# Kernel tuning notes

Hardware: AMD Instinct MI355X
Metric: run time of the kernel (lower is better)

The kernel has to match this reference:

```python
import jax, jax.numpy as jnp
import numpy as np

N_NODES = 32768
N_EDGES = 131072
BATCH = 512
SEQ_LEN = 1000
VOCAB = 26  # vocab_size=25 + 1 padding row
EMB = 128


def _bn(x, g, b):
    # BatchNorm1d forward with batch statistics (training-mode math), eps=1e-5
    m = x.mean(0)
    v = x.var(0)
    return g * (x - m) * jax.lax.rsqrt(v + 1e-5) + b


def _gcn(x, src, dst, W, b, n):
    deg = 1.0 + jax.ops.segment_sum(jnp.ones(src.shape[0], x.dtype), dst, num_segments=n)
    dis = jax.lax.rsqrt(deg)
    xw = x @ W
    msg = xw[src] * (dis[src] * dis[dst])[:, None]
    agg = jax.ops.segment_sum(msg, dst, num_segments=n) + xw * (dis * dis)[:, None]
    return agg + b


def _conv1d(x, k, b, pad):
    # x: [B, C_in, L], k: [C_out, C_in, K]
    y = jax.lax.conv_general_dilated(x, k, (1,), [(pad, pad)],
                                     dimension_numbers=('NCH', 'OIH', 'NCH'))
    return y + b[None, :, None]


def setup_inputs() -> dict:
    key = jax.random.key(0)
    ks = jax.random.split(key, 32)
    f = lambda i, shape, s=0.1: (jax.random.normal(ks[i], shape, dtype=jnp.float32) * s)
    inp = {
        'x': jax.random.normal(ks[0], (N_NODES, 5), dtype=jnp.float32),
        'edge_index': jax.random.randint(ks[1], (2, N_EDGES), 0, N_NODES, dtype=jnp.int32),
        'batch': jnp.sort(jax.random.randint(ks[2], (N_NODES,), 0, BATCH, dtype=jnp.int32)),
        'protein_seq': jax.random.randint(ks[3], (BATCH, SEQ_LEN), 0, VOCAB, dtype=jnp.int32),
        # GCN weights
        'W1': f(4, (5, 64)), 'b1': f(5, (64,)),
        'g1': jnp.ones((64,)), 'bt1': jnp.zeros((64,)),
        'W2': f(6, (64, 128)), 'b2': f(7, (128,)),
        'g2': jnp.ones((128,)), 'bt2': jnp.zeros((128,)),
        'W3': f(8, (128, 128)), 'b3': f(9, (128,)),
        'g3': jnp.ones((128,)), 'bt3': jnp.zeros((128,)),
        # protein embedding (row 0 = padding_idx, zeroed)
        'emb': f(10, (VOCAB, EMB)).at[0].set(0.0),
        # protein convs
        'ck1': f(11, (32, 128, 4)), 'cb1': f(12, (32,)),
        'ck2': f(13, (64, 32, 6)), 'cb2': f(14, (64,)),
        'ck3': f(15, (96, 64, 8)), 'cb3': f(16, (96,)),
        'fw1': f(17, (224, 512)), 'fb1': f(18, (512,)),
        'fw2': f(19, (512, 256)), 'fb2': f(20, (256,)),
        'fw3': f(21, (256, 1)), 'fb3': f(22, (1,)),
    }
    return inp


def reference(x, edge_index, batch, protein_seq,
              W1, b1, g1, bt1, W2, b2, g2, bt2, W3, b3, g3, bt3,
              emb, ck1, cb1, ck2, cb2, ck3, cb3,
              fw1, fb1, fw2, fb2, fw3, fb3):
    src, dst = edge_index[0], edge_index[1]
    relu = jax.nn.relu
    # Drug GNN encoder
    h = relu(_bn(_gcn(x, src, dst, W1, b1, N_NODES), g1, bt1))
    h = relu(_bn(_gcn(h, src, dst, W2, b2, N_NODES), g2, bt2))
    h = relu(_bn(_gcn(h, src, dst, W3, b3, N_NODES), g3, bt3))
    cnt = jax.ops.segment_sum(jnp.ones(N_NODES, h.dtype), batch, num_segments=BATCH)
    drug_emb = jax.ops.segment_sum(h, batch, num_segments=BATCH) / jnp.maximum(cnt, 1.0)[:, None]
    # Protein CNN encoder
    e = emb[protein_seq]                    # [B, L, 128]
    p = jnp.transpose(e, (0, 2, 1))         # [B, 128, L]
    p = relu(_conv1d(p, ck1, cb1, 1))       # [B, 32, 999]
    p = relu(_conv1d(p, ck2, cb2, 2))       # [B, 64, 998]
    p = relu(_conv1d(p, ck3, cb3, 3))       # [B, 96, 997]
    prot_emb = p.max(axis=2)                # [B, 96]
    c = jnp.concatenate([drug_emb, prot_emb], axis=1)  # [B, 224]
    c = relu(c @ fw1 + fb1)
    c = relu(c @ fw2 + fb2)
    out = (c @ fw3 + fb3)[:, 0]             # [B]
    return out
```

## Files before the change

### kernel.cpp

```cpp
#include <hip/hip_runtime.h>

#define NN 32768
#define NE 131072
#define NB 512
#define SL 1000

using bf16x8 = __attribute__((ext_vector_type(8))) short;
using f32x4  = __attribute__((ext_vector_type(4))) float;

static __device__ __forceinline__ unsigned short f2b(float f) {
  union { float f; unsigned u; } x; x.f = f;
  unsigned r = x.u + 0x7fffu + ((x.u >> 16) & 1u);
  return (unsigned short)(r >> 16);
}

static __device__ __forceinline__ void bn_from_raw(float sum, float ssq, float g, float b,
                                                   float& sc, float& sh) {
  float m = sum / 32768.f;
  float v = ssq / 32768.f - m * m;
  sc = g * rsqrtf(v + 1e-5f);
  sh = b - m * sc;
}

__global__ void k_degprep(const int* __restrict__ dst, int* __restrict__ degi,
                          const float* __restrict__ emb, const float* __restrict__ ck1,
                          const float* __restrict__ ck2, const float* __restrict__ ck3,
                          unsigned short* __restrict__ emb_bf, unsigned short* __restrict__ wt1,
                          unsigned short* __restrict__ wt2, unsigned short* __restrict__ wt3) {
  int gid = blockIdx.x * 256 + threadIdx.x;
  atomicAdd(&degi[dst[gid]], 1);
  int idx = gid;
  if (idx < 3328) {
    emb_bf[idx] = f2b(emb[idx]);
  } else if (idx < 3328 + 16384) {
    int i = idx - 3328;
    int kt = i >> 12, co = (i >> 7) & 31, ci = i & 127;
    wt1[i] = f2b(ck1[co * 512 + ci * 4 + kt]);
  } else if (idx < 3328 + 16384 + 12288) {
    int i = idx - 3328 - 16384;
    int kt = i >> 11, co = (i >> 5) & 63, ci = i & 31;
    wt2[i] = f2b(ck2[co * 192 + ci * 6 + kt]);
  } else if (idx < 3328 + 16384 + 12288 + 49152) {
    int i = idx - 3328 - 16384 - 12288;
    int kt = i / 6144, co = (i >> 6) % 96, ci = i & 63;
    wt3[i] = f2b(ck3[co * 512 + ci * 8 + kt]);
  }
}

__global__ void k_scan(const int* __restrict__ degi, int* __restrict__ base,
                       int* __restrict__ cursor, float* __restrict__ dis) {
  __shared__ int part[1024];
  int tid = threadIdx.x;
  int v[32];
  int s = 0;
  int lo = tid * 32;
#pragma unroll
  for (int i = 0; i < 32; ++i) { v[i] = degi[lo + i]; s += v[i]; }
  part[tid] = s;
  __syncthreads();
  for (int off = 1; off < 1024; off <<= 1) {
    int val = (tid >= off) ? part[tid - off] : 0;
    __syncthreads();
    part[tid] += val;
    __syncthreads();
  }
  int run = (tid > 0) ? part[tid - 1] : 0;
#pragma unroll
  for (int i = 0; i < 32; ++i) {
    base[lo + i] = run;
    cursor[lo + i] = run;
    dis[lo + i] = rsqrtf(1.0f + (float)v[i]);
    run += v[i];
  }
  if (tid == 1023) base[NN] = run;
}

__global__ void k_fill(const int* __restrict__ src, const int* __restrict__ dst,
                       int* __restrict__ cursor, unsigned short* __restrict__ csr_src, int E) {
  int e = blockIdx.x * 256 + threadIdx.x;
  if (e < E) {
    int d = dst[e];
    int pos = atomicAdd(&cursor[d], 1);
    csr_src[pos] = (unsigned short)src[e];
  }
}

__launch_bounds__(256)
__global__ void k_gfc1s(const float* __restrict__ x, const float* __restrict__ dis,
                        const int* __restrict__ base, const unsigned short* __restrict__ csr_src,
                        const float* __restrict__ W1, float* __restrict__ out,
                        float* __restrict__ st) {
  __shared__ float sW[5][64];
  __shared__ float a5[256][6];
  __shared__ float red[16][64];
  int tid = threadIdx.x;
  for (int i = tid; i < 320; i += 256) sW[i >> 6][i & 63] = W1[i];
  int n = blockIdx.x * 256 + tid;
  float dn = dis[n];
  float s2 = dn * dn;
  const float* xn = x + (long)n * 5;
  float a0 = xn[0] * s2, a1 = xn[1] * s2, a2 = xn[2] * s2, a3 = xn[3] * s2, a4 = xn[4] * s2;
  int b0 = base[n], b1 = base[n + 1];
  int sNext = (b0 < b1) ? csr_src[b0] : 0;
  for (int j = b0; j < b1; ++j) {
    int s = sNext;
    if (j + 1 < b1) sNext = csr_src[j + 1];
    float coef = dis[s] * dn;
    const float* xs = x + (long)s * 5;
    a0 += xs[0] * coef; a1 += xs[1] * coef; a2 += xs[2] * coef;
    a3 += xs[3] * coef; a4 += xs[4] * coef;
  }
  a5[tid][0] = a0; a5[tid][1] = a1; a5[tid][2] = a2; a5[tid][3] = a3; a5[tid][4] = a4;
  __syncthreads();
  int co = (tid & 15) * 4, strip = tid >> 4;
  float4 s4 = {0.f, 0.f, 0.f, 0.f}, ss4 = {0.f, 0.f, 0.f, 0.f};
  for (int i = 0; i < 16; ++i) {
    int nl = strip * 16 + i;
    long nn = (long)blockIdx.x * 256 + nl;
    float4 acc = {0.f, 0.f, 0.f, 0.f};
#pragma unroll
    for (int ci = 0; ci < 5; ++ci) {
      float av = a5[nl][ci];
      acc.x += av * sW[ci][co];     acc.y += av * sW[ci][co + 1];
      acc.z += av * sW[ci][co + 2]; acc.w += av * sW[ci][co + 3];
    }
    *(float4*)&out[nn * 64 + co] = acc;
    s4.x += acc.x; s4.y += acc.y; s4.z += acc.z; s4.w += acc.w;
    ss4.x += acc.x * acc.x; ss4.y += acc.y * acc.y;
    ss4.z += acc.z * acc.z; ss4.w += acc.w * acc.w;
  }
  *(float4*)&red[strip][co] = s4;
  __syncthreads();
  if (tid < 64) {
    float t = 0.f;
#pragma unroll
    for (int s = 0; s < 16; ++s) t += red[s][tid];
    atomicAdd(&st[tid], t);
  }
  __syncthreads();
  *(float4*)&red[strip][co] = ss4;
  __syncthreads();
  if (tid < 64) {
    float t = 0.f;
#pragma unroll
    for (int s = 0; s < 16; ++s) t += red[s][tid];
    atomicAdd(&st[64 + tid], t);
  }
}

template<int C>
__launch_bounds__(256)
__global__ void k_gbngather(const float* __restrict__ in, const float* __restrict__ dis,
                            const int* __restrict__ base, const unsigned short* __restrict__ csr_src,
                            const float* __restrict__ st, const float* __restrict__ g,
                            const float* __restrict__ bt, float* __restrict__ out) {
  constexpr int TPN = C / 4;
  int t = blockIdx.x * 256 + threadIdx.x;
  int n = t / TPN;
  int c = (t % TPN) * 4;
  float4 sum4 = *(const float4*)&st[c];
  float4 ssq4 = *(const float4*)&st[C + c];
  float4 gg = *(const float4*)&g[c];
  float4 bb = *(const float4*)&bt[c];
  float4 sc4, sh4;
  bn_from_raw(sum4.x, ssq4.x, gg.x, bb.x, sc4.x, sh4.x);
  bn_from_raw(sum4.y, ssq4.y, gg.y, bb.y, sc4.y, sh4.y);
  bn_from_raw(sum4.z, ssq4.z, gg.z, bb.z, sc4.z, sh4.z);
  bn_from_raw(sum4.w, ssq4.w, gg.w, bb.w, sc4.w, sh4.w);
  float dn = dis[n];
  float s2 = dn * dn;
  float4 a = *(const float4*)&in[(long)n * C + c];
  float4 acc;
  acc.x = fmaxf(a.x * sc4.x + sh4.x, 0.f) * s2;
  acc.y = fmaxf(a.y * sc4.y + sh4.y, 0.f) * s2;
  acc.z = fmaxf(a.z * sc4.z + sh4.z, 0.f) * s2;
  acc.w = fmaxf(a.w * sc4.w + sh4.w, 0.f) * s2;
  int b0 = base[n], b1 = base[n + 1];
  int sNext = (b0 < b1) ? csr_src[b0] : 0;
  for (int j = b0; j < b1; ++j) {
    int s = sNext;
    if (j + 1 < b1) sNext = csr_src[j + 1];
    float coef = dis[s] * dn;
    float4 vv = *(const float4*)&in[(long)s * C + c];
    acc.x += fmaxf(vv.x * sc4.x + sh4.x, 0.f) * coef;
    acc.y += fmaxf(vv.y * sc4.y + sh4.y, 0.f) * coef;
    acc.z += fmaxf(vv.z * sc4.z + sh4.z, 0.f) * coef;
    acc.w += fmaxf(vv.w * sc4.w + sh4.w, 0.f) * coef;
  }
  *(float4*)&out[(long)n * C + c] = acc;
}

template<int C_OUT, int K, int TN, bool RELU, bool BIAS, bool STATS>
__launch_bounds__(256)
__global__ void k_fc4(const float* __restrict__ in, const float* __restrict__ W,
                      const float* __restrict__ bias, float* __restrict__ out,
                      float* __restrict__ st, int N) {
  constexpr int CO4 = C_OUT / 4;
  constexpr int GPB = 256 / CO4;
  int g = blockIdx.x * GPB + threadIdx.x / CO4;
  long n0 = (long)g * TN;
  if (!STATS && n0 >= N) return;
  int co = (threadIdx.x % CO4) * 4;
  float4 acc[TN];
  float4 b4 = {0.f, 0.f, 0.f, 0.f};
  if (BIAS) b4 = *(const float4*)&bias[co];
#pragma unroll
  for (int t = 0; t < TN; ++t) acc[t] = b4;
  for (int ci = 0; ci < K; ci += 4) {
    float4 w0 = *(const float4*)&W[(long)(ci + 0) * C_OUT + co];
    float4 w1 = *(const float4*)&W[(long)(ci + 1) * C_OUT + co];
    float4 w2 = *(const float4*)&W[(long)(ci + 2) * C_OUT + co];
    float4 w3 = *(const float4*)&W[(long)(ci + 3) * C_OUT + co];
#pragma unroll
    for (int t = 0; t < TN; ++t) {
      float4 a = *(const float4*)&in[(n0 + t) * K + ci];
      acc[t].x += a.x * w0.x; acc[t].y += a.x * w0.y; acc[t].z += a.x * w0.z; acc[t].w += a.x * w0.w;
      acc[t].x += a.y * w1.x; acc[t].y += a.y * w1.y; acc[t].z += a.y * w1.z; acc[t].w += a.y * w1.w;
      acc[t].x += a.z * w2.x; acc[t].y += a.z * w2.y; acc[t].z += a.z * w2.z; acc[t].w += a.z * w2.w;
      acc[t].x += a.w * w3.x; acc[t].y += a.w * w3.y; acc[t].z += a.w * w3.z; acc[t].w += a.w * w3.w;
    }
  }
  float4 s4 = {0.f, 0.f, 0.f, 0.f}, ss4 = {0.f, 0.f, 0.f, 0.f};
#pragma unroll
  for (int t = 0; t < TN; ++t) {
    float4 o = acc[t];
    if (RELU) {
      o.x = fmaxf(o.x, 0.f); o.y = fmaxf(o.y, 0.f);
      o.z = fmaxf(o.z, 0.f); o.w = fmaxf(o.w, 0.f);
    }
    *(float4*)&out[(n0 + t) * C_OUT + co] = o;
    if (STATS) {
      s4.x += o.x; s4.y += o.y; s4.z += o.z; s4.w += o.w;
      ss4.x += o.x * o.x; ss4.y += o.y * o.y;
      ss4.z += o.z * o.z; ss4.w += o.w * o.w;
    }
  }
  if (STATS) {
    __shared__ float red2[GPB][C_OUT];
    int grp = threadIdx.x / CO4;
    *(float4*)&red2[grp][co] = s4;
    __syncthreads();
    if (threadIdx.x < C_OUT) {
      float t = 0.f;
#pragma unroll
      for (int s = 0; s < GPB; ++s) t += red2[s][threadIdx.x];
      atomicAdd(&st[threadIdx.x], t);
    }
    __syncthreads();
    *(float4*)&red2[grp][co] = ss4;
    __syncthreads();
    if (threadIdx.x < C_OUT) {
      float t = 0.f;
#pragma unroll
      for (int s = 0; s < GPB; ++s) t += red2[s][threadIdx.x];
      atomicAdd(&st[C_OUT + threadIdx.x], t);
    }
  }
}

__launch_bounds__(256)
__global__ void k_reg(const float* __restrict__ cbuf,
                      const float* __restrict__ fw1, const float* __restrict__ fb1,
                      const float* __restrict__ fw2, const float* __restrict__ fb2,
                      const float* __restrict__ fw3, const float* __restrict__ fb3,
                      float* __restrict__ out) {
  __shared__ float cin[224];
  __shared__ float h1[512];
  __shared__ float h2[256];
  __shared__ float red[4];
  int b = blockIdx.x, t = threadIdx.x;
  if (t < 224) cin[t] = cbuf[b * 224 + t];
  __syncthreads();
  {
    float a0 = fb1[t], a1 = fb1[t + 256];
    for (int ci = 0; ci < 224; ++ci) {
      float av = cin[ci];
      a0 += av * fw1[ci * 512 + t];
      a1 += av * fw1[ci * 512 + t + 256];
    }
    h1[t] = fmaxf(a0, 0.f);
    h1[t + 256] = fmaxf(a1, 0.f);
  }
  __syncthreads();
  {
    float a = fb2[t];
    for (int ci = 0; ci < 512; ++ci) a += h1[ci] * fw2[ci * 256 + t];
    h2[t] = fmaxf(a, 0.f);
  }
  __syncthreads();
  {
    float p = h2[t] * fw3[t];
#pragma unroll
    for (int off = 32; off > 0; off >>= 1) p += __shfl_down(p, off, 64);
    if ((t & 63) == 0) red[t >> 6] = p;
    __syncthreads();
    if (t == 0) out[b] = red[0] + red[1] + red[2] + red[3] + fb3[0];
  }
}

__launch_bounds__(256, 3)
__global__ void conv_mfma(const int* __restrict__ seq, const unsigned short* __restrict__ emb_bf,
                          const unsigned short* __restrict__ wt1g, const float* __restrict__ cb1,
                          const unsigned short* __restrict__ wt2g, const float* __restrict__ cb2,
                          const unsigned short* __restrict__ wt3g, const float* __restrict__ cb3,
                          const float* __restrict__ agg, const float* __restrict__ st3,
                          const float* __restrict__ g3, const float* __restrict__ bt3,
                          const int* __restrict__ batch, float* __restrict__ outmax) {
  __shared__ __align__(16) unsigned short s_w[12288];
  __shared__ __align__(16) unsigned short s_c1[4864];
  __shared__ __align__(16) unsigned short s_c2[9216];
  __shared__ int s_tok[152];
  __shared__ int s_max[96];

  int tid = threadIdx.x;
  int b = blockIdx.y;

  if (blockIdx.x == 8) {
    __shared__ int s_lo, s_hi;
    if (tid == 0) {
      int lo = 0, hi = NN;
      while (lo < hi) { int m = (lo + hi) >> 1; if (batch[m] < b) lo = m + 1; else hi = m; }
      s_lo = lo;
      hi = NN;
      while (lo < hi) { int m = (lo + hi) >> 1; if (batch[m] <= b) lo = m + 1; else hi = m; }
      s_hi = lo;
    }
    __syncthreads();
    if (tid < 128) {
      int lo = s_lo, hi = s_hi, c = tid;
      float sc, sh;
      bn_from_raw(st3[c], st3[128 + c], g3[c], bt3[c], sc, sh);
      float s = 0.f;
      for (int n = lo; n < hi; ++n) s += fmaxf(agg[(long)n * 128 + c] * sc + sh, 0.f);
      outmax[b * 224 + c] = s / fmaxf((float)(hi - lo), 1.0f);
    }
    return;
  }

  int t0 = blockIdx.x * 128;

  if (tid < 96) s_max[tid] = 0;
  if (tid < 152) {
    int p = t0 - 6 + tid;
    s_tok[tid] = (p >= 0 && p < SL) ? seq[b * SL + p] : 0;
  }
  if (tid < 128) ((int*)(s_c1 + 144 * 32))[tid] = 0;

  {
    int v0 = tid, v1 = tid + 256;
    *(bf16x8*)&s_w[(v0 >> 4) * 128 + ((((v0 >> 4) ^ v0) & 15) << 3)] = *(const bf16x8*)(wt1g + v0 * 8);
    *(bf16x8*)&s_w[(v1 >> 4) * 128 + ((((v1 >> 4) ^ v1) & 15) << 3)] = *(const bf16x8*)(wt1g + v1 * 8);
  }
  __syncthreads();

  int lane = tid & 63, wave = tid >> 6;
  int l15 = lane & 15, quad = lane >> 4;

  {
    int mt0 = wave, mt1 = wave + 4;
    f32x4 acc0[2], acc1[2], acc2[2];
#pragma unroll
    for (int nt = 0; nt < 2; ++nt) {
      float bv = cb1[nt * 16 + l15];
      acc0[nt] = (f32x4){bv, bv, bv, bv};
      acc1[nt] = (f32x4){bv, bv, bv, bv};
      acc2[nt] = (f32x4){bv, bv, bv, bv};
    }
    for (int kt = 0; kt < 4; ++kt) {
      int bo = (kt & 1) * 4096;
      if (kt < 3) {
        int bo2 = 4096 - bo;
        const unsigned short* wsrc = wt1g + (kt + 1) * 4096;
        int v0 = tid, v1 = tid + 256;
        *(bf16x8*)&s_w[bo2 + (v0 >> 4) * 128 + ((((v0 >> 4) ^ v0) & 15) << 3)] = *(const bf16x8*)(wsrc + v0 * 8);
        *(bf16x8*)&s_w[bo2 + (v1 >> 4) * 128 + ((((v1 >> 4) ^ v1) & 15) << 3)] = *(const bf16x8*)(wsrc + v1 * 8);
      }
      const unsigned short* e0 = emb_bf + s_tok[mt0 * 16 + l15 + kt] * 128 + quad * 8;
      const unsigned short* e1 = emb_bf + s_tok[mt1 * 16 + l15 + kt] * 128 + quad * 8;
#pragma unroll
      for (int cb = 0; cb < 4; ++cb) {
        bf16x8 a0 = *(const bf16x8*)(e0 + cb * 32);
        bf16x8 a1 = *(const bf16x8*)(e1 + cb * 32);
#pragma unroll
        for (int nt = 0; nt < 2; ++nt) {
          bf16x8 bf = *(const bf16x8*)&s_w[bo + (nt * 16 + l15) * 128 + (((cb * 4 + quad) ^ l15) << 3)];
          acc0[nt] = __builtin_amdgcn_mfma_f32_16x16x32_bf16(a0, bf, acc0[nt], 0, 0, 0);
          acc1[nt] = __builtin_amdgcn_mfma_f32_16x16x32_bf16(a1, bf, acc1[nt], 0, 0, 0);
        }
      }
      if (wave == 0) {
        const unsigned short* e2 = emb_bf + s_tok[128 + l15 + kt] * 128 + quad * 8;
#pragma unroll
        for (int cb = 0; cb < 4; ++cb) {
          bf16x8 a2 = *(const bf16x8*)(e2 + cb * 32);
#pragma unroll
          for (int nt = 0; nt < 2; ++nt) {
            bf16x8 bf = *(const bf16x8*)&s_w[bo + (nt * 16 + l15) * 128 + (((cb * 4 + quad) ^ l15) << 3)];
            acc2[nt] = __builtin_amdgcn_mfma_f32_16x16x32_bf16(a2, bf, acc2[nt], 0, 0, 0);
          }
        }
      }
      __syncthreads();
    }
#pragma unroll
    for (int nt = 0; nt < 2; ++nt) {
      int co = nt * 16 + l15;
#pragma unroll
      for (int r = 0; r < 4; ++r) {
        {
          int m = mt0 * 16 + quad * 4 + r;
          int l1 = t0 - 5 + m;
          unsigned short hv = f2b(fmaxf(acc0[nt][r], 0.f));
          s_c1[m * 32 + ((((co >> 3) ^ m) & 3) << 3) + (co & 7)] = (l1 >= 0 && l1 < 999) ? hv : (unsigned short)0;
        }
        {
          int m = mt1 * 16 + quad * 4 + r;
          int l1 = t0 - 5 + m;
          unsigned short hv = f2b(fmaxf(acc1[nt][r], 0.f));
          s_c1[m * 32 + ((((co >> 3) ^ m) & 3) << 3) + (co & 7)] = (l1 >= 0 && l1 < 999) ? hv : (unsigned short)0;
        }
      }
    }
    if (wave == 0) {
#pragma unroll
      for (int nt = 0; nt < 2; ++nt) {
        int co = nt * 16 + l15;
#pragma unroll
        for (int r = 0; r < 4; ++r) {
          int m = 128 + quad * 4 + r;
          int l1 = t0 - 5 + m;
          unsigned short hv = f2b(fmaxf(acc2[nt][r], 0.f));
          s_c1[m * 32 + ((((co >> 3) ^ m) & 3) << 3) + (co & 7)] = (l1 >= 0 && l1 < 999) ? hv : (unsigned short)0;
        }
      }
    }
  }

  {
    bf16x8 w2t[6];
#pragma unroll
    for (int c = 0; c < 6; ++c) w2t[c] = *(const bf16x8*)(wt2g + (c * 256 + tid) * 8);
#pragma unroll
    for (int c = 0; c < 6; ++c) {
      int ch = c * 256 + tid;
      int row = ch >> 2;
      *(bf16x8*)&s_w[row * 32 + (((row ^ ch) & 3) << 3)] = w2t[c];
    }
    __syncthreads();
  }

  {
    int mt0 = wave, mt1 = wave + 4;
    f32x4 acc[2][4];
#pragma unroll
    for (int nt = 0; nt < 4; ++nt) {
      float bv = cb2[nt * 16 + l15];
      acc[0][nt] = (f32x4){bv, bv, bv, bv};
      acc[1][nt] = (f32x4){bv, bv, bv, bv};
    }
    for (int kt = 0; kt < 6; ++kt) {
      int r0 = mt0 * 16 + l15 + kt, r1 = mt1 * 16 + l15 + kt;
      bf16x8 a0 = *(const bf16x8*)&s_c1[r0 * 32 + (((quad ^ r0) & 3) << 3)];
      bf16x8 a1 = *(const bf16x8*)&s_c1[r1 * 32 + (((quad ^ r1) & 3) << 3)];
#pragma unroll
      for (int nt = 0; nt < 4; ++nt) {
        int wr = kt * 64 + nt * 16 + l15;
        bf16x8 bf = *(const bf16x8*)&s_w[wr * 32 + (((quad ^ wr) & 3) << 3)];
        acc[0][nt] = __builtin_amdgcn_mfma_f32_16x16x32_bf16(a0, bf, acc[0][nt], 0, 0, 0);
        acc[1][nt] = __builtin_amdgcn_mfma_f32_16x16x32_bf16(a1, bf, acc[1][nt], 0, 0, 0);
      }
    }
#pragma unroll
    for (int mb = 0; mb < 2; ++mb) {
      int mt = mb ? mt1 : mt0;
#pragma unroll
      for (int nt = 0; nt < 4; ++nt) {
        int co = nt * 16 + l15;
#pragma unroll
        for (int r = 0; r < 4; ++r) {
          int m = mt * 16 + quad * 4 + r;
          int l2 = t0 - 3 + m;
          unsigned short hv = f2b(fmaxf(acc[mb][nt][r], 0.f));
          s_c2[m * 64 + ((((co >> 3) ^ m) & 7) << 3) + (co & 7)] = (l2 >= 0 && l2 < 998) ? hv : (unsigned short)0;
        }
      }
    }
    if (wave == 0) {
      f32x4 acc8[4];
#pragma unroll
      for (int nt = 0; nt < 4; ++nt) {
        float bv = cb2[nt * 16 + l15];
        acc8[nt] = (f32x4){bv, bv, bv, bv};
      }
      for (int kt = 0; kt < 6; ++kt) {
        int r0 = 128 + l15 + kt;
        bf16x8 a0 = *(const bf16x8*)&s_c1[r0 * 32 + (((quad ^ r0) & 3) << 3)];
#pragma unroll
        for (int nt = 0; nt < 4; ++nt) {
          int wr = kt * 64 + nt * 16 + l15;
          bf16x8 bf = *(const bf16x8*)&s_w[wr * 32 + (((quad ^ wr) & 3) << 3)];
          acc8[nt] = __builtin_amdgcn_mfma_f32_16x16x32_bf16(a0, bf, acc8[nt], 0, 0, 0);
        }
      }
#pragma unroll
      for (int nt = 0; nt < 4; ++nt) {
        int co = nt * 16 + l15;
#pragma unroll
        for (int r = 0; r < 4; ++r) {
          int m = 128 + quad * 4 + r;
          int l2 = t0 - 3 + m;
          unsigned short hv = f2b(fmaxf(acc8[nt][r], 0.f));
          s_c2[m * 64 + ((((co >> 3) ^ m) & 7) << 3) + (co & 7)] = (l2 >= 0 && l2 < 998) ? hv : (unsigned short)0;
        }
      }
    }
  }

  {
    bf16x8 w3t[3];
#pragma unroll
    for (int c = 0; c < 3; ++c) w3t[c] = *(const bf16x8*)(wt3g + (c * 256 + tid) * 8);
    __syncthreads();
#pragma unroll
    for (int c = 0; c < 3; ++c) {
      int ch = c * 256 + tid;
      int row = ch >> 3;
      *(bf16x8*)&s_w[row * 64 + (((row ^ ch) & 7) << 3)] = w3t[c];
    }
    __syncthreads();
  }

  {
    int mt0 = wave, mt1 = wave + 4;
    f32x4 acc[2][6];
#pragma unroll
    for (int nt = 0; nt < 6; ++nt) {
      float bv = cb3[nt * 16 + l15];
      acc[0][nt] = (f32x4){bv, bv, bv, bv};
      acc[1][nt] = (f32x4){bv, bv, bv, bv};
    }
    for (int kt = 0; kt < 8; ++kt) {
      bf16x8 w3t[3];
      if (kt < 7) {
#pragma unroll
        for (int c = 0; c < 3; ++c)
          w3t[c] = *(const bf16x8*)(wt3g + ((kt + 1) * 768 + c * 256 + tid) * 8);
      }
      int bo = (kt & 1) * 6144;
      int ra0 = mt0 * 16 + l15 + kt, ra1 = mt1 * 16 + l15 + kt;
#pragma unroll
      for (int cb = 0; cb < 2; ++cb) {
        bf16x8 a0 = *(const bf16x8*)&s_c2[ra0 * 64 + ((((cb * 4 + quad) ^ ra0) & 7) << 3)];
        bf16x8 a1 = *(const bf16x8*)&s_c2[ra1 * 64 + ((((cb * 4 + quad) ^ ra1) & 7) << 3)];
#pragma unroll
        for (int nt = 0; nt < 6; ++nt) {
          int wr = nt * 16 + l15;
          bf16x8 bf = *(const bf16x8*)&s_w[bo + wr * 64 + ((((cb * 4 + quad) ^ wr) & 7) << 3)];
          acc[0][nt] = __builtin_amdgcn_mfma_f32_16x16x32_bf16(a0, bf, acc[0][nt], 0, 0, 0);
          acc[1][nt] = __builtin_amdgcn_mfma_f32_16x16x32_bf16(a1, bf, acc[1][nt], 0, 0, 0);
        }
      }
      if (kt < 7) {
        int bo2 = 6144 - bo;
#pragma unroll
        for (int c = 0; c < 3; ++c) {
          int ch = c * 256 + tid;
          int row = ch >> 3;
          *(bf16x8*)&s_w[bo2 + row * 64 + (((row ^ ch) & 7) << 3)] = w3t[c];
        }
      }
      __syncthreads();
    }
#pragma unroll
    for (int nt = 0; nt < 6; ++nt) {
      int co = nt * 16 + l15;
      float mx = 0.f;
#pragma unroll
      for (int mb = 0; mb < 2; ++mb) {
        int mt = mb ? mt1 : mt0;
#pragma unroll
        for (int r = 0; r < 4; ++r) {
          int l3 = t0 + mt * 16 + quad * 4 + r;
          if (l3 < 997) mx = fmaxf(mx, acc[mb][nt][r]);
        }
      }
      atomicMax(&s_max[co], __float_as_int(mx));
    }
  }
  __syncthreads();
  if (tid < 96) atomicMax((int*)&outmax[b * 224 + 128 + tid], s_max[tid]);
}

extern "C" void kernel_launch(void* const* d_in, const int* in_sizes, int n_in,
                              void* d_out, int out_size, void* d_ws, size_t ws_size,
                              hipStream_t stream) {
  (void)in_sizes; (void)n_in; (void)out_size; (void)ws_size;
  const float* x = (const float*)d_in[0];
  const int* ei = (const int*)d_in[1];
  const int* batch = (const int*)d_in[2];
  const int* seq = (const int*)d_in[3];
  const float* W1 = (const float*)d_in[4];
  const float* g1 = (const float*)d_in[6];
  const float* bt1 = (const float*)d_in[7];
  const float* W2 = (const float*)d_in[8];
  const float* g2 = (const float*)d_in[10];
  const float* bt2 = (const float*)d_in[11];
  const float* W3 = (const float*)d_in[12];
  const float* g3 = (const float*)d_in[14];
  const float* bt3 = (const float*)d_in[15];
  const float* emb = (const float*)d_in[16];
  const float* ck1 = (const float*)d_in[17];
  const float* cb1 = (const float*)d_in[18];
  const float* ck2 = (const float*)d_in[19];
  const float* cb2 = (const float*)d_in[20];
  const float* ck3 = (const float*)d_in[21];
  const float* cb3 = (const float*)d_in[22];
  const float* fw1 = (const float*)d_in[23];
  const float* fb1 = (const float*)d_in[24];
  const float* fw2 = (const float*)d_in[25];
  const float* fb2 = (const float*)d_in[26];
  const float* fw3 = (const float*)d_in[27];
  const float* fb3 = (const float*)d_in[28];
  const int* src = ei;
  const int* dst = ei + NE;

  float* ws = (float*)d_ws;
  float* bufA = ws;
  float* bufB = ws + 4194304;
  float* dis = ws + 8388608;
  float* stats = ws + 8421376;
  float* cbuf = ws + 8422032;
  int* degi = (int*)(ws + 8536720);
  int* base = degi + NN;
  int* cursor = base + NN + 1;
  unsigned short* csr_src = (unsigned short*)(cursor + NN);
  unsigned short* emb_bf = (unsigned short*)(ws + 8700564);
  unsigned short* wt1 = emb_bf + 3328;
  unsigned short* wt2 = wt1 + 16384;
  unsigned short* wt3 = wt2 + 12288;
  float* out = (float*)d_out;

  hipMemsetAsync(stats, 0, (656 + 114688 + 32768) * sizeof(float), stream);

  k_degprep<<<NE / 256, 256, 0, stream>>>(dst, degi, emb, ck1, ck2, ck3, emb_bf, wt1, wt2, wt3);
  k_scan<<<1, 1024, 0, stream>>>(degi, base, cursor, dis);
  k_fill<<<NE / 256, 256, 0, stream>>>(src, dst, cursor, csr_src, NE);

  k_gfc1s<<<NN / 256, 256, 0, stream>>>(x, dis, base, csr_src, W1, bufA, stats);
  k_gbngather<64><<<NN * 16 / 256, 256, 0, stream>>>(bufA, dis, base, csr_src, stats, g1, bt1, bufB);
  k_fc4<128, 64, 4, false, false, true><<<1024, 256, 0, stream>>>(bufB, W2, nullptr, bufA, stats + 128, NN);
  k_gbngather<128><<<NN * 32 / 256, 256, 0, stream>>>(bufA, dis, base, csr_src, stats + 128, g2, bt2, bufB);
  k_fc4<128, 128, 4, false, false, true><<<1024, 256, 0, stream>>>(bufB, W3, nullptr, bufA, stats + 384, NN);

  conv_mfma<<<dim3(9, NB), 256, 0, stream>>>(seq, emb_bf, wt1, cb1, wt2, cb2, wt3, cb3,
                                             bufA, stats + 384, g3, bt3, batch, cbuf);

  k_reg<<<NB, 256, 0, stream>>>(cbuf, fw1, fb1, fw2, fb2, fw3, fb3, out);
}
```

Measured before the change: 431.2 us.

## Precompute embedding-by-conv1 weight table, replace conv1 MFMA with table lookups

Because the first conv runs on embeddings of only 26 tokens, the product of each token embedding with each conv1 tap is precomputed once in the prep kernel as a 26x4x32 fp32 table. Conv1 in the main kernel then sums four table rows per output position instead of running bf16 MFMAs over 128 input channels. This removes conv1 weight staging, MFMA work and syncs from every block, at the cost of a small serial dot-product loop in the prep kernel and gathers from a global table. Precision improves slightly since the table is kept in fp32.

```diff
diff --git a/kernel.cpp b/kernel.cpp
--- a/kernel.cpp
+++ b/kernel.cpp
@@ -26,7 +26,8 @@
                           const float* __restrict__ emb, const float* __restrict__ ck1,
                           const float* __restrict__ ck2, const float* __restrict__ ck3,
                           unsigned short* __restrict__ emb_bf, unsigned short* __restrict__ wt1,
-                          unsigned short* __restrict__ wt2, unsigned short* __restrict__ wt3) {
+                          unsigned short* __restrict__ wt2, unsigned short* __restrict__ wt3,
+                          float* __restrict__ e1) {
   int gid = blockIdx.x * 256 + threadIdx.x;
   atomicAdd(&degi[dst[gid]], 1);
   int idx = gid;
@@ -44,6 +45,14 @@
     int i = idx - 3328 - 16384 - 12288;
     int kt = i / 6144, co = (i >> 6) % 96, ci = i & 63;
     wt3[i] = f2b(ck3[co * 512 + ci * 8 + kt]);
+  } else if (idx < 3328 + 16384 + 12288 + 49152 + 3328) {
+    int i = idx - 81152;
+    int t = i >> 7, kt = (i >> 5) & 3, co = i & 31;
+    const float* er = emb + t * 128;
+    float s = 0.f;
+#pragma unroll 4
+    for (int ci = 0; ci < 128; ++ci) s += er[ci] * ck1[co * 512 + ci * 4 + kt];
+    e1[i] = s;
   }
 }
 
@@ -299,8 +308,8 @@
 }
 
 __launch_bounds__(256, 3)
-__global__ void conv_mfma(const int* __restrict__ seq, const unsigned short* __restrict__ emb_bf,
-                          const unsigned short* __restrict__ wt1g, const float* __restrict__ cb1,
+__global__ void conv_mfma(const int* __restrict__ seq, const float* __restrict__ e1g,
+                          const float* __restrict__ cb1,
                           const unsigned short* __restrict__ wt2g, const float* __restrict__ cb2,
                           const unsigned short* __restrict__ wt3g, const float* __restrict__ cb3,
                           const float* __restrict__ agg, const float* __restrict__ st3,
@@ -347,107 +356,54 @@
   if (tid < 128) ((int*)(s_c1 + 144 * 32))[tid] = 0;
 
   {
-    int v0 = tid, v1 = tid + 256;
-    *(bf16x8*)&s_w[(v0 >> 4) * 128 + ((((v0 >> 4) ^ v0) & 15) << 3)] = *(const bf16x8*)(wt1g + v0 * 8);
-    *(bf16x8*)&s_w[(v1 >> 4) * 128 + ((((v1 >> 4) ^ v1) & 15) << 3)] = *(const bf16x8*)(wt1g + v1 * 8);
-  }
-  __syncthreads();
-
-  int lane = tid & 63, wave = tid >> 6;
-  int l15 = lane & 15, quad = lane >> 4;
-
-  {
-    int mt0 = wave, mt1 = wave + 4;
-    f32x4 acc0[2], acc1[2], acc2[2];
-#pragma unroll
-    for (int nt = 0; nt < 2; ++nt) {
-      float bv = cb1[nt * 16 + l15];
-      acc0[nt] = (f32x4){bv, bv, bv, bv};
-      acc1[nt] = (f32x4){bv, bv, bv, bv};
-      acc2[nt] = (f32x4){bv, bv, bv, bv};
-    }
-    for (int kt = 0; kt < 4; ++kt) {
-      int bo = (kt & 1) * 4096;
-      if (kt < 3) {
-        int bo2 = 4096 - bo;
-        const unsigned short* wsrc = wt1g + (kt + 1) * 4096;
-        int v0 = tid, v1 = tid + 256;
-        *(bf16x8*)&s_w[bo2 + (v0 >> 4) * 128 + ((((v0 >> 4) ^ v0) & 15) << 3)] = *(const bf16x8*)(wsrc + v0 * 8);
-        *(bf16x8*)&s_w[bo2 + (v1 >> 4) * 128 + ((((v1 >> 4) ^ v1) & 15) << 3)] = *(const bf16x8*)(wsrc + v1 * 8);
-      }
-      const unsigned short* e0 = emb_bf + s_tok[mt0 * 16 + l15 + kt] * 128 + quad * 8;
-      const unsigned short* e1 = emb_bf + s_tok[mt1 * 16 + l15 + kt] * 128 + quad * 8;
-#pragma unroll
-      for (int cb = 0; cb < 4; ++cb) {
-        bf16x8 a0 = *(const bf16x8*)(e0 + cb * 32);
-        bf16x8 a1 = *(const bf16x8*)(e1 + cb * 32);
-#pragma unroll
-        for (int nt = 0; nt < 2; ++nt) {
-          bf16x8 bf = *(const bf16x8*)&s_w[bo + (nt * 16 + l15) * 128 + (((cb * 4 + quad) ^ l15) << 3)];
-          acc0[nt] = __builtin_amdgcn_mfma_f32_16x16x32_bf16(a0, bf, acc0[nt], 0, 0, 0);
-          acc1[nt] = __builtin_amdgcn_mfma_f32_16x16x32_bf16(a1, bf, acc1[nt], 0, 0, 0);
-        }
-      }
-      if (wave == 0) {
-        const unsigned short* e2 = emb_bf + s_tok[128 + l15 + kt] * 128 + quad * 8;
-#pragma unroll
-        for (int cb = 0; cb < 4; ++cb) {
-          bf16x8 a2 = *(const bf16x8*)(e2 + cb * 32);
-#pragma unroll
-          for (int nt = 0; nt < 2; ++nt) {
-            bf16x8 bf = *(const bf16x8*)&s_w[bo + (nt * 16 + l15) * 128 + (((cb * 4 + quad) ^ l15) << 3)];
-            acc2[nt] = __builtin_amdgcn_mfma_f32_16x16x32_bf16(a2, bf, acc2[nt], 0, 0, 0);
-          }
-        }
-      }
-      __syncthreads();
-    }
-#pragma unroll
-    for (int nt = 0; nt < 2; ++nt) {
-      int co = nt * 16 + l15;
-#pragma unroll
-      for (int r = 0; r < 4; ++r) {
-        {
-          int m = mt0 * 16 + quad * 4 + r;
-          int l1 = t0 - 5 + m;
-          unsigned short hv = f2b(fmaxf(acc0[nt][r], 0.f));
-          s_c1[m * 32 + ((((co >> 3) ^ m) & 3) << 3) + (co & 7)] = (l1 >= 0 && l1 < 999) ? hv : (unsigned short)0;
-        }
-        {
-          int m = mt1 * 16 + quad * 4 + r;
-          int l1 = t0 - 5 + m;
-          unsigned short hv = f2b(fmaxf(acc1[nt][r], 0.f));
-          s_c1[m * 32 + ((((co >> 3) ^ m) & 3) << 3) + (co & 7)] = (l1 >= 0 && l1 < 999) ? hv : (unsigned short)0;
-        }
-      }
-    }
-    if (wave == 0) {
-#pragma unroll
-      for (int nt = 0; nt < 2; ++nt) {
-        int co = nt * 16 + l15;
-#pragma unroll
-        for (int r = 0; r < 4; ++r) {
-          int m = 128 + quad * 4 + r;
-          int l1 = t0 - 5 + m;
-          unsigned short hv = f2b(fmaxf(acc2[nt][r], 0.f));
-          s_c1[m * 32 + ((((co >> 3) ^ m) & 3) << 3) + (co & 7)] = (l1 >= 0 && l1 < 999) ? hv : (unsigned short)0;
-        }
-      }
-    }
-  }
-
-  {
-    bf16x8 w2t[6];
-#pragma unroll
-    for (int c = 0; c < 6; ++c) w2t[c] = *(const bf16x8*)(wt2g + (c * 256 + tid) * 8);
 #pragma unroll
     for (int c = 0; c < 6; ++c) {
       int ch = c * 256 + tid;
       int row = ch >> 2;
-      *(bf16x8*)&s_w[row * 32 + (((row ^ ch) & 3) << 3)] = w2t[c];
-    }
-    __syncthreads();
-  }
+      *(bf16x8*)&s_w[row * 32 + (((row ^ ch) & 3) << 3)] = *(const bf16x8*)(wt2g + ch * 8);
+    }
+  }
+  __syncthreads();
+
+  int lane = tid & 63, wave = tid >> 6;
+  int l15 = lane & 15, quad = lane >> 4;
+
+  {
+    bool edge = (blockIdx.x == 0) || (blockIdx.x == 7);
+#pragma unroll
+    for (int pass = 0; pass < 2; ++pass) {
+      int m = (pass == 0) ? (tid >> 1) : (128 + (tid >> 1));
+      bool act = (pass == 0) || (tid < 32);
+      if (act) {
+        int co0 = (tid & 1) * 16;
+        f32x4 a4[4];
+#pragma unroll
+        for (int q = 0; q < 4; ++q) a4[q] = *(const f32x4*)&cb1[co0 + q * 4];
+#pragma unroll
+        for (int kt = 0; kt < 4; ++kt) {
+          const float* e = e1g + s_tok[m + kt] * 128 + kt * 32 + co0;
+#pragma unroll
+          for (int q = 0; q < 4; ++q) {
+            f32x4 v = *(const f32x4*)&e[q * 4];
+            a4[q][0] += v[0]; a4[q][1] += v[1]; a4[q][2] += v[2]; a4[q][3] += v[3];
+          }
+        }
+        int l1 = t0 - 5 + m;
+        bool ok = !edge || (l1 >= 0 && l1 < 999);
+#pragma unroll
+        for (int q = 0; q < 4; ++q) {
+#pragma unroll
+          for (int e2 = 0; e2 < 4; e2 += 2) {
+            int co = co0 + q * 4 + e2;
+            unsigned lo = ok ? (unsigned)f2b(fmaxf(a4[q][e2], 0.f)) : 0u;
+            unsigned hi = ok ? (unsigned)f2b(fmaxf(a4[q][e2 + 1], 0.f)) : 0u;
+            *(unsigned*)&s_c1[m * 32 + ((((co >> 3) ^ m) & 3) << 3) + (co & 7)] = lo | (hi << 16);
+          }
+        }
+      }
+    }
+  }
+  __syncthreads();
 
   {
     int mt0 = wave, mt1 = wave + 4;
@@ -638,11 +594,12 @@
   unsigned short* wt1 = emb_bf + 3328;
   unsigned short* wt2 = wt1 + 16384;
   unsigned short* wt3 = wt2 + 12288;
+  float* e1 = ws + 8741140;
   float* out = (float*)d_out;
 
   hipMemsetAsync(stats, 0, (656 + 114688 + 32768) * sizeof(float), stream);
 
-  k_degprep<<<NE / 256, 256, 0, stream>>>(dst, degi, emb, ck1, ck2, ck3, emb_bf, wt1, wt2, wt3);
+  k_degprep<<<NE / 256, 256, 0, stream>>>(dst, degi, emb, ck1, ck2, ck3, emb_bf, wt1, wt2, wt3, e1);
   k_scan<<<1, 1024, 0, stream>>>(degi, base, cursor, dis);
   k_fill<<<NE / 256, 256, 0, stream>>>(src, dst, cursor, csr_src, NE);
 
@@ -652,7 +609,7 @@
   k_gbngather<128><<<NN * 32 / 256, 256, 0, stream>>>(bufA, dis, base, csr_src, stats + 128, g2, bt2, bufB);
   k_fc4<128, 128, 4, false, false, true><<<1024, 256, 0, stream>>>(bufB, W3, nullptr, bufA, stats + 384, NN);
 
-  conv_mfma<<<dim3(9, NB), 256, 0, stream>>>(seq, emb_bf, wt1, cb1, wt2, cb2, wt3, cb3,
+  conv_mfma<<<dim3(9, NB), 256, 0, stream>>>(seq, e1, cb1, wt2, cb2, wt3, cb3,
                                              bufA, stats + 384, g3, bt3, batch, cbuf);
 
   k_reg<<<NB, 256, 0, stream>>>(cbuf, fw1, fb1, fw2, fb2, fw3, fb3, out);
```

Measured after the change: 408.3 us. 5.3% less time.
